# Kernel optimization log

Hardware: AMD Instinct MI355X
Metric: run time of the kernel (lower is better)

## Reference

```python
import jax, jax.numpy as jnp
from jax import lax
import numpy as np

B, DIM, H, W = 1, 48, 192, 192
HEADS, K, DIL = 2, 7, 3
HD = DIM // HEADS
HID = int(DIM * 2.66)  # 127 (Restormer GEGLU hidden)
EPS = 1e-5


def _window_starts(L, Kk, D):
    # NATTEN window-start rule: keep phase i % D, shift window inside bounds.
    s = np.zeros(L, dtype=np.int32)
    for i in range(L):
        if D <= 1:
            st = max(i - Kk // 2, 0)
            if i + Kk // 2 >= L:
                st = L - Kk
        else:
            st = i - (Kk // 2) * D
            if st < 0:
                st = i % D
            elif i + (Kk // 2) * D >= L:
                imodd = i % D
                a = (L // D) * D
                b = L - a
                if imodd < b:
                    st = L - b + imodd - 2 * (Kk // 2) * D
                else:
                    st = a + imodd - Kk * D
        s[i] = st
    return s


def _nbr_tables(L, Kk, D):
    st = _window_starts(L, Kk, D)
    idx = st[:, None] + np.arange(Kk)[None, :] * D          # [L, K] absolute neighbor idx
    pb = (st - np.arange(L)) // D                            # signed offset of window start (in dilation units)
    pb = pb[:, None] + (Kk - 1) + np.arange(Kk)[None, :]     # [L, K] rpb index in [0, 2K-2]
    return jnp.asarray(idx), jnp.asarray(pb)

IH, PBH = _nbr_tables(H, K, DIL)
IW, PBW = _nbr_tables(W, K, DIL)


def layernorm(x, w, b):  # channel LN on NCHW (WithBias, biased var)
    mu = x.mean(1, keepdims=True)
    var = ((x - mu) ** 2).mean(1, keepdims=True)
    return (x - mu) / jnp.sqrt(var + EPS) * w[None, :, None, None] + b[None, :, None, None]


def na2d(x, qkv_w, qkv_b, rpb, proj_w, proj_b):
    # x: NCHW -> BHWC
    t = x.transpose(0, 2, 3, 1)
    qkv = t @ qkv_w.T + qkv_b                                # [B,H,W,3*DIM]
    qkv = qkv.reshape(B, H, W, 3, HEADS, HD)
    q, k, v = qkv[:, :, :, 0], qkv[:, :, :, 1], qkv[:, :, :, 2]
    q = q * (HD ** -0.5)
    # gather dilated 7x7 neighborhoods: [B, H, K, W, K, heads, hd]
    kn = k[:, IH[:, :, None, None], IW[None, None, :, :]]
    vn = v[:, IH[:, :, None, None], IW[None, None, :, :]]
    attn = jnp.einsum('bijnc,bixjync->bijnxy', q, kn)        # [B,H,W,heads,K,K]
    bias = rpb[:, PBH][:, :, :, PBW]                         # [heads,H,K,W,K]
    attn = attn + bias.transpose(1, 3, 0, 2, 4)
    attn = jax.nn.softmax(attn.reshape(B, H, W, HEADS, K * K), axis=-1)
    attn = attn.reshape(B, H, W, HEADS, K, K)
    out = jnp.einsum('bijnxy,bixjync->bijnc', attn, vn).reshape(B, H, W, DIM)
    out = out @ proj_w.T + proj_b
    return out.transpose(0, 3, 1, 2)


def chan_mod(x, eca_w):  # ECA-style gate: GAP -> 1D conv over channels -> sigmoid
    p = x.mean((2, 3))                                       # [B,C]
    y = lax.conv_general_dilated(p[:, None, :], eca_w[None, None, :], (1,), [(3, 3)],
                                 dimension_numbers=('NCH', 'OIH', 'NCH'))[:, 0, :]
    return jax.nn.sigmoid(y)[:, :, None, None]


def ffn(x, w_in, w_dw, w_out):  # conv-GEGLU
    t = jnp.einsum('bchw,oc->bohw', x, w_in)                 # 1x1: DIM -> 2*HID
    t = lax.conv_general_dilated(t, w_dw, (1, 1), [(1, 1), (1, 1)],
                                 feature_group_count=2 * HID,
                                 dimension_numbers=('NCHW', 'OIHW', 'NCHW'))
    x1, x2 = t[:, :HID], t[:, HID:]
    g = jax.nn.gelu(x1, approximate=False) * x2
    return jnp.einsum('bchw,oc->bohw', g, w_out)             # 1x1: HID -> DIM


def setup_inputs() -> dict:
    key = jax.random.key(0)
    ks = jax.random.split(key, 10)
    d = {
        'x': jax.random.normal(ks[0], (B, DIM, H, W), jnp.float32),
        'ln1_w': jnp.ones((DIM,), jnp.float32),
        'ln1_b': jnp.zeros((DIM,), jnp.float32),
        'qkv_w': jax.random.normal(ks[1], (3 * DIM, DIM), jnp.float32) * 0.05,
        'qkv_b': jnp.zeros((3 * DIM,), jnp.float32),
        'rpb': jax.random.normal(ks[2], (HEADS, 2 * K - 1, 2 * K - 1), jnp.float32) * 0.02,
        'proj_w': jax.random.normal(ks[3], (DIM, DIM), jnp.float32) * 0.05,
        'proj_b': jnp.zeros((DIM,), jnp.float32),
        'eca_w': jax.random.normal(ks[4], (7,), jnp.float32) * 0.1,
        'ln2_w': jnp.ones((DIM,), jnp.float32),
        'ln2_b': jnp.zeros((DIM,), jnp.float32),
        'w_in': jax.random.normal(ks[5], (2 * HID, DIM), jnp.float32) * 0.05,
        'w_dw': jax.random.normal(ks[6], (2 * HID, 1, 3, 3), jnp.float32) * 0.05,
        'w_out': jax.random.normal(ks[7], (DIM, HID), jnp.float32) * 0.05,
    }
    return d


def reference(x, ln1_w, ln1_b, qkv_w, qkv_b, rpb, proj_w, proj_b, eca_w,
              ln2_w, ln2_b, w_in, w_dw, w_out):
    xn1 = layernorm(x, ln1_w, ln1_b)
    x = x + na2d(xn1, qkv_w, qkv_b, rpb, proj_w, proj_b) * chan_mod(xn1, eca_w)
    x = x + ffn(layernorm(x, ln2_w, ln2_b), w_in, w_dw, w_out)
    return x
```

## Files before the change

### kernel.cpp

```cpp
#include <hip/hip_runtime.h>
#include <hip/hip_bf16.h>
#include <math.h>

#define HW_ (192*192)
#define Wd 192
#define HIDc 127
#define NBLK1 (HW_/64)

#define O_LN1W 0
#define O_QKVW 96
#define O_QKVB 7008
#define O_RPB  7152
#define O_PROJW 7490
#define O_PROJB 9794
#define O_ECA  9842
#define O_LN2W 9849
#define O_WIN  9946
#define O_WDW  22138
#define O_WOUT 24424
#define WTS_LEN 30520

typedef unsigned short ushort_t;
typedef _Float16 half2_t __attribute__((ext_vector_type(2)));
typedef float f32x2 __attribute__((ext_vector_type(2)));

__device__ __forceinline__ float b2f(__hip_bfloat16 v){ return __bfloat162float(v); }
__device__ __forceinline__ float u2f(ushort_t h){ return __uint_as_float(((unsigned)h)<<16); }
__device__ __forceinline__ ushort_t f2u(float f){
    __hip_bfloat16 h = __float2bfloat16(f);
    union { __hip_bfloat16 b; ushort_t u; } c; c.b = h; return c.u;
}
__device__ __forceinline__ void up2(unsigned u, float& a, float& b){
    a = __uint_as_float(u << 16);
    b = __uint_as_float(u & 0xffff0000u);
}
__device__ __forceinline__ unsigned pkh2(float a, float b){
    half2_t h; h[0] = (_Float16)a; h[1] = (_Float16)b;
    union { half2_t h; unsigned u; } c; c.h = h; return c.u;
}
__device__ __forceinline__ half2_t u2h2(unsigned u){
    union { unsigned u; half2_t h; } c; c.u = u; return c.h;
}
__device__ __forceinline__ float dot2h(half2_t a, half2_t b, float c){
    return c + (float)a[0]*(float)b[0] + (float)a[1]*(float)b[1];
}
__device__ __forceinline__ float dot48p(const f32x2* __restrict__ wr,
                                        const f32x2* __restrict__ xp){
    f32x2 a0 = {0.f, 0.f}, a1 = {0.f, 0.f};
    #pragma unroll
    for (int d = 0; d < 24; d += 2){
        a0 += wr[d]     * xp[d];
        a1 += wr[d + 1] * xp[d + 1];
    }
    f32x2 a = a0 + a1;
    return a[0] + a[1];
}

__device__ __forceinline__ int wstart(int i){
    if (i < 9) return i % 3;
    if (i >= 183) return 171 + (i % 3);
    return i - 9;
}

__global__ void convert_kernel(
    const void* p0, const void* p1, const void* p2, const void* p3,
    const void* p4, const void* p5, const void* p6, const void* p7,
    const void* p8, const void* p9, const void* p10, const void* p11,
    const void* p12, const ushort_t* __restrict__ xu, int* __restrict__ mode_out,
    float* __restrict__ wts, float* __restrict__ woutTf)
{
    __shared__ int sbad;
    if (threadIdx.x == 0) sbad = 0;
    __syncthreads();
    {
        unsigned u = xu[2*threadIdx.x];
        float f = __uint_as_float(u << 16);
        if (!(fabsf(f) < 100.f)) atomicAdd(&sbad, 1);
    }
    __syncthreads();
    const int md = (sbad > 16) ? 1 : 0;
    if (blockIdx.x == 0 && threadIdx.x == 0) mode_out[0] = md;

    const void* ps[13] = {p0,p1,p2,p3,p4,p5,p6,p7,p8,p9,p10,p11,p12};
    const int sz[13]  = {48,48,6912,144,338,2304,48,7,48,48,12192,2286,6096};
    const int off[13] = {O_LN1W,48,O_QKVW,O_QKVB,O_RPB,O_PROJW,O_PROJB,O_ECA,
                         O_LN2W,9897,O_WIN,O_WDW,O_WOUT};
    int b = blockIdx.x;
    if (b == 14){
        if (md){
            const float* s = (const float*)p12;
            for (int i = threadIdx.x; i < 6096; i += 256){
                int c = i / 48, o = i - c*48;
                woutTf[i] = s[o*127 + c];
            }
        } else {
            const ushort_t* s = (const ushort_t*)p12;
            for (int i = threadIdx.x; i < 6096; i += 256){
                int c = i / 48, o = i - c*48;
                woutTf[i] = u2f(s[o*127 + c]);
            }
        }
        return;
    }
    if (b >= 13) return;
    int n = sz[b];
    float* dst = wts + off[b];
    if (md){
        const float* s = (const float*)ps[b];
        for (int i = threadIdx.x; i < n; i += 256) dst[i] = s[i];
    } else {
        const __hip_bfloat16* s = (const __hip_bfloat16*)ps[b];
        for (int i = threadIdx.x; i < n; i += 256) dst[i] = b2f(s[i]);
    }
}

__global__ __launch_bounds__(384) void ln1qkv_kernel(
    const void* __restrict__ x, const int* __restrict__ mode,
    const float* __restrict__ wts,
    ushort_t* __restrict__ q, ushort_t* __restrict__ k, ushort_t* __restrict__ v,
    float* __restrict__ chpart)
{
    __shared__ float sx[64*49];

    const int tid  = threadIdx.x;
    const int px_l = tid & 63;
    const int r6   = __builtin_amdgcn_readfirstlane(tid >> 6);
    const int p0   = blockIdx.x * 64;
    const int p    = p0 + px_l;

    if (mode[0]){
        const float* xf = (const float*)x;
        for (int idx = tid; idx < 64*48; idx += 384){
            int c = idx >> 6, pl = idx & 63;
            sx[pl*49 + c] = xf[c*HW_ + p0 + pl];
        }
    } else {
        const __hip_bfloat16* xb = (const __hip_bfloat16*)x;
        for (int idx = tid; idx < 64*48; idx += 384){
            int c = idx >> 6, pl = idx & 63;
            sx[pl*49 + c] = b2f(xb[c*HW_ + p0 + pl]);
        }
    }
    __syncthreads();

    f32x2 xp[24];
    float mu = 0.f;
    #pragma unroll
    for (int c = 0; c < 24; c++){
        xp[c][0] = sx[px_l*49 + 2*c];
        xp[c][1] = sx[px_l*49 + 2*c + 1];
        mu += xp[c][0] + xp[c][1];
    }
    mu *= (1.f/48.f);
    float var = 0.f;
    #pragma unroll
    for (int c = 0; c < 24; c++){
        float d0 = xp[c][0]-mu, d1 = xp[c][1]-mu;
        var += d0*d0 + d1*d1;
    }
    var *= (1.f/48.f);
    float rs = rsqrtf(var + 1e-5f);
    #pragma unroll
    for (int c = 0; c < 24; c++){
        xp[c][0] = (xp[c][0]-mu)*rs*wts[O_LN1W + 2*c]   + wts[O_LN1W + 48 + 2*c];
        xp[c][1] = (xp[c][1]-mu)*rs*wts[O_LN1W + 2*c+1] + wts[O_LN1W + 48 + 2*c+1];
    }

    if (tid < 64){
        #pragma unroll
        for (int c = 0; c < 48; c++){
            float s = xp[c>>1][c&1];
            s += __shfl_xor(s, 1);  s += __shfl_xor(s, 2);  s += __shfl_xor(s, 4);
            s += __shfl_xor(s, 8);  s += __shfl_xor(s, 16); s += __shfl_xor(s, 32);
            if (tid == 0) chpart[blockIdx.x*48 + c] = s;
        }
    }

    const int rbase = r6 * 24;
    const float scale = (r6 < 2) ? 0.20412414523193154f : 1.0f;
    float ov[24];
    #pragma unroll 4
    for (int ro = 0; ro < 24; ro++){
        int r = rbase + ro;
        float acc = wts[O_QKVB + r]
                  + dot48p((const f32x2*)(wts + O_QKVW + r*48), xp);
        ov[ro] = acc * scale;
    }

    unsigned int pk[12];
    #pragma unroll
    for (int d = 0; d < 12; d++)
        pk[d] = pkh2(ov[2*d], ov[2*d+1]);
    ushort_t* tp = (r6 >> 1) == 0 ? q : ((r6 >> 1) == 1 ? k : v);
    uint4* dst4 = (uint4*)(tp + (size_t)(r6 & 1)*(HW_*24) + (size_t)p*24);
    dst4[0] = make_uint4(pk[0], pk[1], pk[2],  pk[3]);
    dst4[1] = make_uint4(pk[4], pk[5], pk[6],  pk[7]);
    dst4[2] = make_uint4(pk[8], pk[9], pk[10], pk[11]);
}

__global__ __launch_bounds__(256) void gatefuse_kernel(
    const float* __restrict__ chpart, const float* __restrict__ wts,
    float* __restrict__ gate)
{
    __shared__ float sm[48];
    const int t = threadIdx.x;
    if (t < 192){
        const int ch = t >> 2, qq = t & 3;
        float acc = 0.f;
        #pragma unroll 4
        for (int b = qq; b < NBLK1; b += 4)
            acc += chpart[b*48 + ch];
        acc += __shfl_xor(acc, 1);
        acc += __shfl_xor(acc, 2);
        if (qq == 0) sm[ch] = acc * (1.f / (float)HW_);
    }
    __syncthreads();
    if (t < 48){
        float a = 0.f;
        for (int kk = 0; kk < 7; kk++){
            int cc = t + kk - 3;
            if (cc >= 0 && cc < 48) a += wts[O_ECA + kk] * sm[cc];
        }
        gate[t] = 1.f / (1.f + expf(-a));
    }
}

__global__ __launch_bounds__(256) void attnfuse_kernel(
    const ushort_t* __restrict__ q, const ushort_t* __restrict__ k,
    const ushort_t* __restrict__ v, const float* __restrict__ wts,
    const float* __restrict__ gate,
    const void* __restrict__ x, const int* __restrict__ mode,
    float* __restrict__ x2, ushort_t* __restrict__ tout)
{
    __shared__ float srpb[338];
    __shared__ float sa[64*49];

    const int bx   = (int)blockIdx.x;
    const int tile = (bx & 7) * (NBLK1 >> 3) + (bx >> 3);

    const int tid = threadIdx.x;
    for (int i0 = tid; i0 < 338; i0 += 256) srpb[i0] = wts[O_RPB + i0];
    __syncthreads();

    const int parity = tid & 1;
    const int head   = (tid >> 1) & 1;
    const int px_l   = tid >> 2;
    const int px     = tile * 64 + px_l;
    const int i = px / Wd, j = px % Wd;
    const int sti = wstart(i), stj = wstart(j);
    const int pbi = (sti - i) / 3 + 6;
    const int pbj = (stj - j) / 3 + 6;
    const float* rpb = srpb + head*169;
    const size_t hplane = (size_t)head * (HW_*24);

    half2_t qh[12];
    {
        const uint4* qp = (const uint4*)(q + hplane + (size_t)px*24);
        uint4 q0 = qp[0], q1 = qp[1], q2 = qp[2];
        qh[0]=u2h2(q0.x); qh[1]=u2h2(q0.y); qh[2] =u2h2(q0.z); qh[3] =u2h2(q0.w);
        qh[4]=u2h2(q1.x); qh[5]=u2h2(q1.y); qh[6] =u2h2(q1.z); qh[7] =u2h2(q1.w);
        qh[8]=u2h2(q2.x); qh[9]=u2h2(q2.y); qh[10]=u2h2(q2.z); qh[11]=u2h2(q2.w);
    }

    float s = 0.f;
    float acc[24];
    #pragma unroll
    for (int c = 0; c < 24; c++) acc[c] = 0.f;

    #pragma unroll 5
    for (int tt = 0; tt < 25; tt++){
        int n = 2*tt + parity;
        const bool inval = (n > 48);
        if (inval) n = 48;
        int xx = (n * 147) >> 10;
        int yy = n - 7*xx;
        int ii = sti + 3*xx, jj = stj + 3*yy;
        const size_t nb = hplane + (size_t)(ii*Wd + jj)*24;
        const uint4* kp = (const uint4*)(k + nb);
        const uint4* vp = (const uint4*)(v + nb);
        uint4 K0 = kp[0], K1 = kp[1], K2 = kp[2];
        uint4 V0 = vp[0], V1 = vp[1], V2 = vp[2];
        float d = 0.f;
        d = dot2h(u2h2(K0.x), qh[0],  d);
        d = dot2h(u2h2(K0.y), qh[1],  d);
        d = dot2h(u2h2(K0.z), qh[2],  d);
        d = dot2h(u2h2(K0.w), qh[3],  d);
        d = dot2h(u2h2(K1.x), qh[4],  d);
        d = dot2h(u2h2(K1.y), qh[5],  d);
        d = dot2h(u2h2(K1.z), qh[6],  d);
        d = dot2h(u2h2(K1.w), qh[7],  d);
        d = dot2h(u2h2(K2.x), qh[8],  d);
        d = dot2h(u2h2(K2.y), qh[9],  d);
        d = dot2h(u2h2(K2.z), qh[10], d);
        d = dot2h(u2h2(K2.w), qh[11], d);
        float sc = d + rpb[(pbi+xx)*13 + (pbj+yy)];
        sc = fminf(sc, 80.f);
        if (inval) sc = -1e30f;
        float p = __expf(sc);
        s += p;
        half2_t vv;
        vv=u2h2(V0.x); acc[0] +=p*(float)vv[0]; acc[1] +=p*(float)vv[1];
        vv=u2h2(V0.y); acc[2] +=p*(float)vv[0]; acc[3] +=p*(float)vv[1];
        vv=u2h2(V0.z); acc[4] +=p*(float)vv[0]; acc[5] +=p*(float)vv[1];
        vv=u2h2(V0.w); acc[6] +=p*(float)vv[0]; acc[7] +=p*(float)vv[1];
        vv=u2h2(V1.x); acc[8] +=p*(float)vv[0]; acc[9] +=p*(float)vv[1];
        vv=u2h2(V1.y); acc[10]+=p*(float)vv[0]; acc[11]+=p*(float)vv[1];
        vv=u2h2(V1.z); acc[12]+=p*(float)vv[0]; acc[13]+=p*(float)vv[1];
        vv=u2h2(V1.w); acc[14]+=p*(float)vv[0]; acc[15]+=p*(float)vv[1];
        vv=u2h2(V2.x); acc[16]+=p*(float)vv[0]; acc[17]+=p*(float)vv[1];
        vv=u2h2(V2.y); acc[18]+=p*(float)vv[0]; acc[19]+=p*(float)vv[1];
        vv=u2h2(V2.z); acc[20]+=p*(float)vv[0]; acc[21]+=p*(float)vv[1];
        vv=u2h2(V2.w); acc[22]+=p*(float)vv[0]; acc[23]+=p*(float)vv[1];
    }

    s += __shfl_xor(s, 1);
    const float inv = 1.f / s;
    float mg[12];
    #pragma unroll
    for (int c = 0; c < 12; c++){
        float mine   = parity ? acc[12+c] : acc[c];
        float theirs = parity ? acc[c]    : acc[12+c];
        mg[c] = (mine + __shfl_xor(theirs, 1)) * inv;
    }
    {
        float* dst = sa + px_l*49 + head*24 + parity*12;
        #pragma unroll
        for (int c = 0; c < 12; c++) dst[c] = mg[c];
    }
    __syncthreads();

    const int px_l2 = tid & 63;
    const int og    = __builtin_amdgcn_readfirstlane(tid >> 6);
    const int px2   = tile * 64 + px_l2;

    f32x2 ar[24];
    #pragma unroll
    for (int c = 0; c < 24; c++){
        ar[c][0] = sa[px_l2*49 + 2*c];
        ar[c][1] = sa[px_l2*49 + 2*c + 1];
    }
    __syncthreads();

    const float* xf = (const float*)x;
    const __hip_bfloat16* xb = (const __hip_bfloat16*)x;
    const int md = mode[0];
    const int ob = og * 12;
    #pragma unroll 2
    for (int oo = 0; oo < 12; oo++){
        int o = ob + oo;
        float accp = wts[O_PROJB + o]
                   + dot48p((const f32x2*)(wts + O_PROJW + o*48), ar);
        float res = md ? xf[o*HW_ + px2] : b2f(xb[o*HW_ + px2]);
        float xv = res + accp * gate[o];
        x2[o*HW_ + px2] = xv;
        sa[px_l2*49 + o] = xv;
    }
    __syncthreads();

    f32x2 xp[24];
    float mu = 0.f;
    #pragma unroll
    for (int c = 0; c < 24; c++){
        xp[c][0] = sa[px_l2*49 + 2*c];
        xp[c][1] = sa[px_l2*49 + 2*c + 1];
        mu += xp[c][0] + xp[c][1];
    }
    mu *= (1.f/48.f);
    float var = 0.f;
    #pragma unroll
    for (int c = 0; c < 24; c++){
        float d0 = xp[c][0]-mu, d1 = xp[c][1]-mu;
        var += d0*d0 + d1*d1;
    }
    var *= (1.f/48.f);
    float rs = rsqrtf(var + 1e-5f);
    #pragma unroll
    for (int c = 0; c < 24; c++){
        xp[c][0] = (xp[c][0]-mu)*rs*wts[O_LN2W + 2*c]   + wts[O_LN2W + 48 + 2*c];
        xp[c][1] = (xp[c][1]-mu)*rs*wts[O_LN2W + 2*c+1] + wts[O_LN2W + 48 + 2*c+1];
    }

    const int base = og * 64;
    for (int t2 = 0; t2 < 64; t2 += 2){
        int o0 = base + t2;
        if (o0 >= 254) break;
        float accA = dot48p((const f32x2*)(wts + O_WIN + o0*48), xp);
        float accB = dot48p((const f32x2*)(wts + O_WIN + min(o0+1,253)*48), xp);
        tout[(size_t)o0*HW_ + px2] = f2u(accA);
        if (o0+1 < 254) tout[(size_t)(o0+1)*HW_ + px2] = f2u(accB);
    }
}

__global__ __launch_bounds__(256) void dw_kernel(
    const ushort_t* __restrict__ t, const float* __restrict__ wts,
    ushort_t* __restrict__ g)
{
    const int ch = blockIdx.y;
    const int pp = (blockIdx.x * 256 + threadIdx.x) * 4;
    const int i  = pp / Wd, j = pp % Wd;
    float w1[9], w2[9];
    #pragma unroll
    for (int s2 = 0; s2 < 9; s2++){
        w1[s2] = wts[O_WDW + ch*9 + s2];
        w2[s2] = wts[O_WDW + (ch+HIDc)*9 + s2];
    }
    const ushort_t* t1 = t + (size_t)ch * HW_;
    const ushort_t* t2 = t + (size_t)(ch+HIDc) * HW_;
    float a10=0.f,a11=0.f,a12=0.f,a13=0.f;
    float a20=0.f,a21=0.f,a22=0.f,a23=0.f;
    #pragma unroll
    for (int di = 0; di < 3; di++){
        int ii = i + di - 1;
        if (ii < 0 || ii >= 192) continue;
        int base = ii*Wd + j;
        float wa = w1[di*3], wb = w1[di*3+1], wc = w1[di*3+2];
        {
            uint2 mm = *(const uint2*)(t1 + base);
            float c0,c1,c2,c3; up2(mm.x,c0,c1); up2(mm.y,c2,c3);
            float cm = (j > 0)     ? u2f(t1[base-1]) : 0.f;
            float cp = (j+4 < Wd)  ? u2f(t1[base+4]) : 0.f;
            a10 += wa*cm + wb*c0 + wc*c1;
            a11 += wa*c0 + wb*c1 + wc*c2;
            a12 += wa*c1 + wb*c2 + wc*c3;
            a13 += wa*c2 + wb*c3 + wc*cp;
        }
        wa = w2[di*3]; wb = w2[di*3+1]; wc = w2[di*3+2];
        {
            uint2 mm = *(const uint2*)(t2 + base);
            float c0,c1,c2,c3; up2(mm.x,c0,c1); up2(mm.y,c2,c3);
            float cm = (j > 0)     ? u2f(t2[base-1]) : 0.f;
            float cp = (j+4 < Wd)  ? u2f(t2[base+4]) : 0.f;
            a20 += wa*cm + wb*c0 + wc*c1;
            a21 += wa*c0 + wb*c1 + wc*c2;
            a22 += wa*c1 + wb*c2 + wc*c3;
            a23 += wa*c2 + wb*c3 + wc*cp;
        }
    }
    const float RS2 = 0.70710678118654752f;
    float g0 = a10 * 0.5f * (1.f + erff(a10 * RS2)) * a20;
    float g1 = a11 * 0.5f * (1.f + erff(a11 * RS2)) * a21;
    float g2 = a12 * 0.5f * (1.f + erff(a12 * RS2)) * a22;
    float g3 = a13 * 0.5f * (1.f + erff(a13 * RS2)) * a23;
    uint2 pk;
    pk.x = (unsigned)f2u(g0) | ((unsigned)f2u(g1) << 16);
    pk.y = (unsigned)f2u(g2) | ((unsigned)f2u(g3) << 16);
    *(uint2*)(g + (size_t)ch*HW_ + pp) = pk;
}

__global__ __launch_bounds__(128) void pw2_kernel(
    const ushort_t* __restrict__ g, const float* __restrict__ woutTf,
    const float* __restrict__ x2, void* __restrict__ outv,
    const int* __restrict__ mode)
{
    const int ob = blockIdx.y * 12;
    const int p  = blockIdx.x * 128 + threadIdx.x;
    f32x2 acc2[6];
    #pragma unroll
    for (int d = 0; d < 6; d++) acc2[d] = (f32x2){0.f, 0.f};
    #pragma unroll 4
    for (int c = 0; c < 127; c++){
        float gv = u2f(g[(size_t)c*HW_ + p]);
        f32x2 gv2; gv2[0] = gv; gv2[1] = gv;
        const f32x2* w2 = (const f32x2*)(woutTf + c*48 + ob);
        #pragma unroll
        for (int d = 0; d < 6; d++) acc2[d] += w2[d] * gv2;
    }
    if (mode[0]){
        float* out = (float*)outv;
        #pragma unroll
        for (int o = 0; o < 12; o++){
            int oc = ob + o;
            out[(size_t)oc*HW_ + p] = x2[(size_t)oc*HW_ + p] + acc2[o>>1][o&1];
        }
    } else {
        __hip_bfloat16* out = (__hip_bfloat16*)outv;
        #pragma unroll
        for (int o = 0; o < 12; o++){
            int oc = ob + o;
            out[(size_t)oc*HW_ + p] =
                __float2bfloat16(x2[(size_t)oc*HW_ + p] + acc2[o>>1][o&1]);
        }
    }
}

extern "C" void kernel_launch(void* const* d_in, const int* in_sizes, int n_in,
                              void* d_out, int out_size, void* d_ws, size_t ws_size,
                              hipStream_t stream)
{
    (void)in_sizes; (void)n_in; (void)out_size;

    char* ws = (char*)d_ws;
    ushort_t* q    = (ushort_t*)(ws);
    ushort_t* k    = (ushort_t*)(ws + 3538944);
    ushort_t* v    = (ushort_t*)(ws + 7077888);
    float*    x2   = (float*)   (ws + 10616832);
    ushort_t* t    = (ushort_t*)(ws + 17694720);
    ushort_t* g    = (ushort_t*)(ws);
    float*    gate = (float*)   (ws + 36421632);
    int*      mode = (int*)     (ws + 36421824);
    float*    wts  = (float*)   (ws + 36421840);
    float*    chpart=(float*)   (ws + 36543920);
    float*    woutTf = (float*) (ws + 36654512);

    size_t need = 36654512 + 24384;
    if (ws_size < need) return;

    convert_kernel<<<15, 256, 0, stream>>>(
        d_in[1], d_in[2], d_in[3], d_in[4], d_in[5], d_in[6], d_in[7],
        d_in[8], d_in[9], d_in[10], d_in[11], d_in[12], d_in[13],
        (const ushort_t*)d_in[0], mode, wts, woutTf);

    ln1qkv_kernel<<<dim3(NBLK1), 384, 0, stream>>>(d_in[0], mode, wts,
                                                   q, k, v, chpart);
    gatefuse_kernel<<<1, 256, 0, stream>>>(chpart, wts, gate);
    attnfuse_kernel<<<dim3(NBLK1), 256, 0, stream>>>(q, k, v, wts, gate,
                                                     d_in[0], mode, x2, t);
    dw_kernel<<<dim3(HW_/1024, 127), 256, 0, stream>>>(t, wts, g);
    pw2_kernel<<<dim3(HW_/128, 4), 128, 0, stream>>>(g, woutTf, x2, d_out, mode);
}
```

Measured before the change: 232.8 us.

## Split attention neighbors across four lanes per pixel-head with 32-pixel tiles

The fused attention kernel now assigns four threads per pixel-head, each covering about a quarter of the 49 neighbors, instead of two threads per pixel-head. Blocks handle 32 pixels and twice as many blocks are launched. Partial sums are combined with butterfly shuffles. Each thread's serial loop gets shorter and the grid gains parallelism. The cost is more shuffle traffic (48 shuffles per thread), more blocks each reloading the RPB table, and thread groups in the projection/FFN stage that cover fewer outputs with less reuse.

```diff
diff --git a/kernel.cpp b/kernel.cpp
--- a/kernel.cpp
+++ b/kernel.cpp
@@ -6,6 +6,7 @@
 #define Wd 192
 #define HIDc 127
 #define NBLK1 (HW_/64)
+#define NTILE2 (HW_/32)
 
 #define O_LN1W 0
 #define O_QKVW 96
@@ -233,19 +234,19 @@
     float* __restrict__ x2, ushort_t* __restrict__ tout)
 {
     __shared__ float srpb[338];
-    __shared__ float sa[64*49];
+    __shared__ float sa[32*49];
 
     const int bx   = (int)blockIdx.x;
-    const int tile = (bx & 7) * (NBLK1 >> 3) + (bx >> 3);
+    const int tile = (bx & 7) * (NTILE2 >> 3) + (bx >> 3);
 
     const int tid = threadIdx.x;
     for (int i0 = tid; i0 < 338; i0 += 256) srpb[i0] = wts[O_RPB + i0];
     __syncthreads();
 
-    const int parity = tid & 1;
-    const int head   = (tid >> 1) & 1;
-    const int px_l   = tid >> 2;
-    const int px     = tile * 64 + px_l;
+    const int p4    = tid & 3;
+    const int head  = (tid >> 2) & 1;
+    const int px_l  = tid >> 3;
+    const int px    = tile * 32 + px_l;
     const int i = px / Wd, j = px % Wd;
     const int sti = wstart(i), stj = wstart(j);
     const int pbi = (sti - i) / 3 + 6;
@@ -267,11 +268,11 @@
     #pragma unroll
     for (int c = 0; c < 24; c++) acc[c] = 0.f;
 
-    #pragma unroll 5
-    for (int tt = 0; tt < 25; tt++){
-        int n = 2*tt + parity;
-        const bool inval = (n > 48);
-        if (inval) n = 48;
+    #pragma unroll 4
+    for (int tt = 0; tt < 13; tt++){
+        int n = 4*tt + p4;
+        const bool bad = (n > 48);
+        if (bad) n = 48;
         int xx = (n * 147) >> 10;
         int yy = n - 7*xx;
         int ii = sti + 3*xx, jj = stj + 3*yy;
@@ -295,7 +296,7 @@
         d = dot2h(u2h2(K2.w), qh[11], d);
         float sc = d + rpb[(pbi+xx)*13 + (pbj+yy)];
         sc = fminf(sc, 80.f);
-        if (inval) sc = -1e30f;
+        if (bad) sc = -1e30f;
         float p = __expf(sc);
         s += p;
         half2_t vv;
@@ -314,24 +315,34 @@
     }
 
     s += __shfl_xor(s, 1);
-    const float inv = 1.f / s;
-    float mg[12];
-    #pragma unroll
-    for (int c = 0; c < 12; c++){
-        float mine   = parity ? acc[12+c] : acc[c];
-        float theirs = parity ? acc[c]    : acc[12+c];
-        mg[c] = (mine + __shfl_xor(theirs, 1)) * inv;
+    s += __shfl_xor(s, 2);
+    #pragma unroll
+    for (int c = 0; c < 24; c++){
+        acc[c] += __shfl_xor(acc[c], 1);
+        acc[c] += __shfl_xor(acc[c], 2);
     }
     {
-        float* dst = sa + px_l*49 + head*24 + parity*12;
-        #pragma unroll
-        for (int c = 0; c < 12; c++) dst[c] = mg[c];
-    }
-    __syncthreads();
-
-    const int px_l2 = tid & 63;
-    const int og    = __builtin_amdgcn_readfirstlane(tid >> 6);
-    const int px2   = tile * 64 + px_l2;
+        const float inv = 1.f / s;
+        float* dst = sa + px_l*49 + head*24;
+        if (p4 == 0){
+            #pragma unroll
+            for (int c = 0; c < 6; c++) dst[c] = acc[c] * inv;
+        } else if (p4 == 1){
+            #pragma unroll
+            for (int c = 0; c < 6; c++) dst[6 + c] = acc[6 + c] * inv;
+        } else if (p4 == 2){
+            #pragma unroll
+            for (int c = 0; c < 6; c++) dst[12 + c] = acc[12 + c] * inv;
+        } else {
+            #pragma unroll
+            for (int c = 0; c < 6; c++) dst[18 + c] = acc[18 + c] * inv;
+        }
+    }
+    __syncthreads();
+
+    const int px_l2 = tid & 31;
+    const int grp   = tid >> 5;
+    const int px2   = tile * 32 + px_l2;
 
     f32x2 ar[24];
     #pragma unroll
@@ -344,9 +355,9 @@
     const float* xf = (const float*)x;
     const __hip_bfloat16* xb = (const __hip_bfloat16*)x;
     const int md = mode[0];
-    const int ob = og * 12;
-    #pragma unroll 2
-    for (int oo = 0; oo < 12; oo++){
+    const int ob = grp * 6;
+    #pragma unroll
+    for (int oo = 0; oo < 6; oo++){
         int o = ob + oo;
         float accp = wts[O_PROJB + o]
                    + dot48p((const f32x2*)(wts + O_PROJW + o*48), ar);
@@ -380,8 +391,8 @@
         xp[c][1] = (xp[c][1]-mu)*rs*wts[O_LN2W + 2*c+1] + wts[O_LN2W + 48 + 2*c+1];
     }
 
-    const int base = og * 64;
-    for (int t2 = 0; t2 < 64; t2 += 2){
+    const int base = grp * 32;
+    for (int t2 = 0; t2 < 32; t2 += 2){
         int o0 = base + t2;
         if (o0 >= 254) break;
         float accA = dot48p((const f32x2*)(wts + O_WIN + o0*48), xp);
@@ -513,8 +524,8 @@
     ln1qkv_kernel<<<dim3(NBLK1), 384, 0, stream>>>(d_in[0], mode, wts,
                                                    q, k, v, chpart);
     gatefuse_kernel<<<1, 256, 0, stream>>>(chpart, wts, gate);
-    attnfuse_kernel<<<dim3(NBLK1), 256, 0, stream>>>(q, k, v, wts, gate,
-                                                     d_in[0], mode, x2, t);
+    attnfuse_kernel<<<dim3(NTILE2), 256, 0, stream>>>(q, k, v, wts, gate,
+                                                      d_in[0], mode, x2, t);
     dw_kernel<<<dim3(HW_/1024, 127), 256, 0, stream>>>(t, wts, g);
     pw2_kernel<<<dim3(HW_/128, 4), 128, 0, stream>>>(g, woutTf, x2, d_out, mode);
 }
```

Result: slower. 265.2 us (+13.9%).
